# Performance work log

Hardware: AMD Instinct MI355X
Metric: run time of the kernel (lower is better)

Reference implementation:

```python
import jax, jax.numpy as jnp
import numpy as np

B, N, G, H, A = 128, 49, 4096, 1024, 1024  # batch, regions, global feat dim, hidden, attn dim


def setup_inputs() -> dict:
    key = jax.random.key(0)
    ks = jax.random.split(key, 11)
    def w(k, shape, fan_in):
        return jax.random.normal(k, shape, jnp.float32) * (1.0 / np.sqrt(fan_in))
    return {
        "global_features": jax.random.normal(ks[0], (B, N, G), jnp.float32),
        "s_t": jax.random.normal(ks[1], (B, H), jnp.float32),
        "cov_a": jax.random.uniform(ks[2], (B, N, 1), jnp.float32),
        "W_g": w(ks[3], (G, G), G),
        "b_g": jnp.zeros((G,), jnp.float32),
        "W_gs": w(ks[4], (G, H), G),
        "b_gs": jnp.zeros((H,), jnp.float32),
        "W_h": w(ks[5], (H, A), H),
        "W_s": w(ks[6], (H, A), H),
        "W_c": w(ks[7], (1, A), 1),
        "v": w(ks[8], (A,), A),
    }


def reference(global_features, s_t, cov_a, W_g, b_g, W_gs, b_gs, W_h, W_s, W_c, v):
    # g_star = Linear(G->G) -> Linear(G->H) applied to region features  [B,N,H]
    g1 = jnp.einsum('bng,gk->bnk', global_features, W_g) + b_g
    g_star = jnp.einsum('bng,gh->bnh', g1, W_gs) + b_gs
    # additive (Bahdanau) energies: e = tanh(W_h g* + W_s s_t + W_c cov)  [B,N,A]
    e = jnp.tanh(
        jnp.einsum('bnh,ha->bna', g_star, W_h)
        + (s_t @ W_s)[:, None, :]
        + cov_a @ W_c
    )
    scores = jnp.einsum('bna,a->bn', e, v)          # [B,N]
    alpha = jax.nn.softmax(scores, axis=-1)          # attention over regions
    c_img = jnp.einsum('bn,bnh->bh', alpha, g_star)  # weighted sum context [B,H]
    return c_img
```

## Files before the change

kernel.cpp:

```cpp
#include <hip/hip_runtime.h>
#include <cstdint>
#include <cstddef>

typedef __bf16 bf16;
typedef __bf16 bf16x8 __attribute__((ext_vector_type(8)));
typedef __bf16 bf16v4 __attribute__((ext_vector_type(4)));
typedef float  f32x4  __attribute__((ext_vector_type(4)));

#define PB   128
#define PN   49
#define PG   4096
#define PH   1024
#define PA   1024
#define PM1  (PB * PN)

__global__ __launch_bounds__(256) void detect_kernel(
    const unsigned short* __restrict__ raw, int* __restrict__ flag)
{
    __shared__ int cnt;
    if (threadIdx.x == 0) cnt = 0;
    __syncthreads();
    unsigned short u = raw[threadIdx.x];
    float x = __uint_as_float(((unsigned int)u) << 16);
    float a = fabsf(x);
    atomicAdd(&cnt, (a >= 1e-7f && a <= 128.f) ? 1 : 0);
    __syncthreads();
    if (threadIdx.x == 0) flag[0] = (cnt >= 200) ? 1 : 0;
}

__device__ __forceinline__ float ldin(const void* p, size_t i, bool in32) {
    return in32 ? ((const float*)p)[i] : (float)((const bf16*)p)[i];
}

__device__ __forceinline__ void ldx8(const void* x, size_t k0, bool in32, float* xv) {
    if (in32) {
        f32x4 lo = *(const f32x4*)((const float*)x + k0);
        f32x4 hi = *(const f32x4*)((const float*)x + k0 + 4);
#pragma unroll
        for (int j = 0; j < 4; ++j) { xv[j] = lo[j]; xv[4 + j] = hi[j]; }
    } else {
        bf16x8 v = *(const bf16x8*)((const bf16*)x + k0);
#pragma unroll
        for (int j = 0; j < 8; ++j) xv[j] = (float)v[j];
    }
}

__global__ __launch_bounds__(256) void cvt_kernel(
    const void* __restrict__ in, const int* __restrict__ flag,
    bf16* __restrict__ out, size_t total)
{
    const bool in32 = (flag[0] == 0);
    const size_t stride = (size_t)gridDim.x * 256 * 8;
    for (size_t i = ((size_t)blockIdx.x * 256 + threadIdx.x) * 8; i < total; i += stride) {
        bf16x8 o;
        if (in32) {
            f32x4 lo = *(const f32x4*)((const float*)in + i);
            f32x4 hi = *(const f32x4*)((const float*)in + i + 4);
#pragma unroll
            for (int j = 0; j < 4; ++j) { o[j] = (bf16)lo[j]; o[4 + j] = (bf16)hi[j]; }
        } else {
            o = *(const bf16x8*)((const bf16*)in + i);
        }
        *(bf16x8*)(out + i) = o;
    }
}

template <int BF16OUT>
__global__ __launch_bounds__(256, 2) void gemm_kernel(
    const bf16* __restrict__ A, const bf16* __restrict__ Bt0,
    float* __restrict__ Cf, bf16* __restrict__ Cb,
    int M, int N, int K, int kTilesPerSplit)
{
    __shared__ __align__(16) bf16 lds[2 * 128 * 64];
    bf16* As  = lds;
    bf16* Bs0 = lds + 128 * 64;

    const int gx = gridDim.x, gy = gridDim.y;
    const int nwg = gx * gy * (int)gridDim.z;
    int flat = blockIdx.x + gx * (blockIdx.y + gy * blockIdx.z);
    {
        const int q8 = nwg >> 3, r8 = nwg & 7;
        const int xcd = flat & 7, sub = flat >> 3;
        flat = (xcd < r8 ? xcd * (q8 + 1) : r8 * (q8 + 1) + (xcd - r8) * q8) + sub;
    }
    const int bx  = flat % gx;
    const int byz = flat / gx;
    const int by  = byz % gy;
    const int bz  = byz / gy;

    const int tid  = threadIdx.x;
    const int m0   = by * 128;
    const int n0   = bx * 128;
    const int kt0  = bz * kTilesPerSplit;

    const int wave = tid >> 6;
    const int lane = tid & 63;
    const int wm   = (wave >> 1) * 64;
    const int wn   = (wave & 1) * 64;
    const int lm   = lane & 15;
    const int q    = lane >> 4;

    f32x4 acc[4][4];
#pragma unroll
    for (int i = 0; i < 4; ++i)
#pragma unroll
        for (int j = 0; j < 4; ++j) acc[i][j] = (f32x4)0.0f;

    for (int kt = 0; kt < kTilesPerSplit; ++kt) {
        const int k0 = (kt0 + kt) * 64;
#pragma unroll
        for (int it = 0; it < 4; ++it) {
            int p   = it * 256 + tid;
            int row = p >> 3;
            int lc  = ((p & 7) - row) & 7;
            size_t offB = (size_t)(n0 + row) * K + k0 + lc * 8;
            __builtin_amdgcn_global_load_lds((void*)(Bt0 + offB), (void*)(Bs0 + p * 8), 16, 0, 0);
            size_t offA = (size_t)(m0 + row) * K + k0 + lc * 8;
            __builtin_amdgcn_global_load_lds((void*)(A + offA), (void*)(As + p * 8), 16, 0, 0);
        }
        __syncthreads();

#pragma unroll
        for (int s = 0; s < 2; ++s) {
            bf16x8 af[4], bf0[4];
            const int c = s * 4 + q;
#pragma unroll
            for (int mi = 0; mi < 4; ++mi) {
                int row  = wm + mi * 16 + lm;
                int slot = row * 8 + ((c + row) & 7);
                af[mi] = *(const bf16x8*)(As + slot * 8);
            }
#pragma unroll
            for (int ni = 0; ni < 4; ++ni) {
                int row  = wn + ni * 16 + lm;
                int slot = row * 8 + ((c + row) & 7);
                bf0[ni] = *(const bf16x8*)(Bs0 + slot * 8);
            }
#pragma unroll
            for (int mi = 0; mi < 4; ++mi)
#pragma unroll
                for (int ni = 0; ni < 4; ++ni)
                    acc[mi][ni] = __builtin_amdgcn_mfma_f32_16x16x32_bf16(
                        af[mi], bf0[ni], acc[mi][ni], 0, 0, 0);
        }
        __syncthreads();
    }

#pragma unroll
    for (int mi = 0; mi < 4; ++mi)
#pragma unroll
        for (int ni = 0; ni < 4; ++ni)
#pragma unroll
            for (int r = 0; r < 4; ++r) {
                int row = m0 + wm + mi * 16 + q * 4 + r;
                int col = n0 + wn + ni * 16 + lm;
                if (BF16OUT)
                    Cb[(size_t)bz * M * N + (size_t)row * N + col] = (bf16)acc[mi][ni][r];
                else
                    Cf[(size_t)bz * M * N + (size_t)row * N + col] = acc[mi][ni][r];
            }
}

__global__ __launch_bounds__(256) void transpose_kernel(
    const void* __restrict__ in, const int* __restrict__ flag,
    bf16* __restrict__ out, int R, int C)
{
    __shared__ bf16 tile[64][65];
    const bool in32 = (flag[0] == 0);
    const int r0 = blockIdx.y * 64, c0 = blockIdx.x * 64;
    const int tx = threadIdx.x & 15, ty = threadIdx.x >> 4;
#pragma unroll
    for (int it = 0; it < 4; ++it) {
        int r = it * 16 + ty;
        size_t base = (size_t)(r0 + r) * C + c0 + tx * 4;
        if (in32) {
            f32x4 v = *(const f32x4*)((const float*)in + base);
#pragma unroll
            for (int i = 0; i < 4; ++i) tile[r][tx * 4 + i] = (bf16)v[i];
        } else {
            bf16v4 v = *(const bf16v4*)((const bf16*)in + base);
#pragma unroll
            for (int i = 0; i < 4; ++i) tile[r][tx * 4 + i] = v[i];
        }
    }
    __syncthreads();
#pragma unroll
    for (int it = 0; it < 4; ++it) {
        int c = it * 16 + ty;
        bf16v4 v;
#pragma unroll
        for (int i = 0; i < 4; ++i) v[i] = tile[tx * 4 + i][c];
        *(bf16v4*)(out + (size_t)(c0 + c) * R + r0 + tx * 4) = v;
    }
}

__global__ __launch_bounds__(256) void reduce4_kernel(
    const bf16* __restrict__ in, bf16* __restrict__ out, size_t n)
{
    size_t i = ((size_t)blockIdx.x * 256 + threadIdx.x) * 8;
    float s[8] = {0,0,0,0,0,0,0,0};
#pragma unroll
    for (int p = 0; p < 4; ++p) {
        bf16x8 v = *(const bf16x8*)(in + (size_t)p * n + i);
#pragma unroll
        for (int j = 0; j < 8; ++j) s[j] += (float)v[j];
    }
    bf16x8 o;
#pragma unroll
    for (int j = 0; j < 8; ++j) o[j] = (bf16)s[j];
    *(bf16x8*)(out + i) = o;
}

__global__ __launch_bounds__(256) void rowdot_kernel(
    const void* __restrict__ x, const bf16* __restrict__ Wt,
    const void* __restrict__ addv, const int* __restrict__ flag, int xMode,
    float* __restrict__ y, int K)
{
    const bool raw32 = (flag[0] == 0);
    const bool x32   = (xMode == 0) || raw32;
    const int wave = threadIdx.x >> 6, lane = threadIdx.x & 63;
    const int c = blockIdx.x * 4 + wave;
    float s = 0.f;
    for (int k0 = lane * 8; k0 < K; k0 += 512) {
        bf16x8 w = *(const bf16x8*)(Wt + (size_t)c * K + k0);
        float xv[8];
        ldx8(x, (size_t)k0, x32, xv);
#pragma unroll
        for (int j = 0; j < 8; ++j) s += xv[j] * (float)w[j];
    }
#pragma unroll
    for (int off = 32; off; off >>= 1) s += __shfl_down(s, off);
    if (lane == 0) {
        float a = addv ? ldin(addv, c, raw32) : 0.f;
        y[c] = s + a;
    }
}

__global__ __launch_bounds__(256) void scores_kernel(
    const bf16* __restrict__ tP, const float* __restrict__ sprojP,
    const float* __restrict__ tbias, const void* __restrict__ cov,
    const void* __restrict__ Wc, const void* __restrict__ v,
    const int* __restrict__ flag, float* __restrict__ sc)
{
    const bool in32 = (flag[0] == 0);
    const int n = blockIdx.x, b = blockIdx.y, tid = threadIdx.x;
    __shared__ float red[4];
    const size_t trow = (size_t)(b * PN + n) * PA;
    const float cv = ldin(cov, b * PN + n, in32);
    float s = 0.f;
#pragma unroll
    for (int i = 0; i < 4; ++i) {
        int a = tid + i * 256;
        float tv = 0.f;
#pragma unroll
        for (int p = 0; p < 2; ++p)
            tv += (float)tP[(size_t)p * ((size_t)PM1 * PA) + trow + a];
        float sp = 0.f;
#pragma unroll
        for (int p = 0; p < 4; ++p)
            sp += sprojP[(size_t)p * (PB * PA) + (size_t)b * PA + a];
        s += ldin(v, a, in32) * tanhf(tv + sp + tbias[a] + cv * ldin(Wc, a, in32));
    }
#pragma unroll
    for (int off = 32; off; off >>= 1) s += __shfl_down(s, off);
    if ((tid & 63) == 0) red[tid >> 6] = s;
    __syncthreads();
    if (tid == 0) sc[b * PN + n] = red[0] + red[1] + red[2] + red[3];
}

__global__ __launch_bounds__(256) void context_kernel(
    const float* __restrict__ sc, const bf16* __restrict__ gstar,
    const float* __restrict__ cbias, const int* __restrict__ flag,
    void* __restrict__ out)
{
    const int b = blockIdx.x, tid = threadIdx.x;
    const int h = tid * 4;
    float e[PN];
    float mx = -1e30f;
    for (int n = 0; n < PN; ++n) mx = fmaxf(mx, sc[b * PN + n]);
    float sum = 0.f;
    for (int n = 0; n < PN; ++n) { e[n] = expf(sc[b * PN + n] - mx); sum += e[n]; }
    const float inv = 1.f / sum;
    f32x4 cb = *(const f32x4*)(cbias + h);
    float acc[4] = {cb[0], cb[1], cb[2], cb[3]};
    for (int n = 0; n < PN; ++n) {
        float al = e[n] * inv;
        bf16v4 g = *(const bf16v4*)(gstar + (size_t)(b * PN + n) * PH + h);
#pragma unroll
        for (int j = 0; j < 4; ++j) acc[j] += al * (float)g[j];
    }
    if (flag[0]) {
        bf16v4 o;
#pragma unroll
        for (int j = 0; j < 4; ++j) o[j] = (bf16)acc[j];
        *(bf16v4*)((bf16*)out + (size_t)b * PH + h) = o;
    } else {
        f32x4 o;
#pragma unroll
        for (int j = 0; j < 4; ++j) o[j] = acc[j];
        *(f32x4*)((float*)out + (size_t)b * PH + h) = o;
    }
}

extern "C" void kernel_launch(void* const* d_in, const int* in_sizes, int n_in,
                              void* d_out, int out_size, void* d_ws, size_t ws_size,
                              hipStream_t stream)
{
    const void* GF  = d_in[0];
    const void* s_t = d_in[1];
    const void* cov = d_in[2];
    const void* Wg  = d_in[3];
    const void* bg  = d_in[4];
    const void* Wgs = d_in[5];
    const void* bgs = d_in[6];
    const void* Wh  = d_in[7];
    const void* Ws  = d_in[8];
    const void* Wc  = d_in[9];
    const void* v   = d_in[10];
    (void)in_sizes; (void)n_in; (void)out_size; (void)ws_size;

    const size_t MB = 1u << 20;
    char* W = (char*)d_ws;
    bf16*  GFb    = (bf16*) (W + 0);
    bf16*  g_star = (bf16*) (W + 0);
    int*   flag   = (int*)  (W + 52 * MB);
    float* tbias  = (float*)(W + 52 * MB + 4096);
    float* cbias  = (float*)(W + 52 * MB + 8192);
    float* sc     = (float*)(W + 52 * MB + 12288);
    bf16*  s_tb   = (bf16*) (W + 52 * MB + 262144);
    bf16*  WsT    = (bf16*) (W + 53 * MB);
    bf16*  WhT    = (bf16*) (W + 55 * MB);
    float* sprojP = (float*)(W + 57 * MB);
    bf16*  WgsT   = (bf16*) (W + 59 * MB);
    bf16*  WggsT  = (bf16*) (W + 59 * MB);
    bf16*  WggsP  = (bf16*) (W + 67 * MB);
    bf16*  gP     = (bf16*) (W + 67 * MB);
    bf16*  t2P    = (bf16*) (W + 67 * MB);
    bf16*  Wgb    = (bf16*) (W + 100 * MB);

    dim3 blk(256);

    detect_kernel<<<dim3(1), blk, 0, stream>>>((const unsigned short*)GF, flag);

    cvt_kernel<<<dim3(2048), blk, 0, stream>>>(GF, flag, GFb, (size_t)PM1 * PG);
    cvt_kernel<<<dim3(2048), blk, 0, stream>>>(Wg, flag, Wgb, (size_t)PG * PG);
    cvt_kernel<<<dim3(64), blk, 0, stream>>>(s_t, flag, s_tb, (size_t)PB * PH);
    transpose_kernel<<<dim3(PH / 64, PG / 64), blk, 0, stream>>>(Wgs, flag, WgsT, PG, PH);
    transpose_kernel<<<dim3(PA / 64, PH / 64), blk, 0, stream>>>(Wh, flag, WhT, PH, PA);
    transpose_kernel<<<dim3(PA / 64, PH / 64), blk, 0, stream>>>(Ws, flag, WsT, PH, PA);

    rowdot_kernel<<<dim3(PH / 4), blk, 0, stream>>>(bg, WgsT, bgs, flag, 1, cbias, PG);
    rowdot_kernel<<<dim3(PA / 4), blk, 0, stream>>>(cbias, WhT, nullptr, flag, 0, tbias, PH);

    gemm_kernel<1><<<dim3(PG / 128, PH / 128, 4), blk, 0, stream>>>(
        WgsT, Wgb, nullptr, WggsP, PH, PG, PG, (PG / 64) / 4);
    reduce4_kernel<<<dim3((PH * PG) / 2048), blk, 0, stream>>>(
        WggsP, WggsT, (size_t)PH * PG);

    gemm_kernel<1><<<dim3(PH / 128, PM1 / 128, 4), blk, 0, stream>>>(
        GFb, WggsT, nullptr, gP, PM1, PH, PG, (PG / 64) / 4);
    reduce4_kernel<<<dim3((PM1 * PH) / 2048), blk, 0, stream>>>(
        gP, g_star, (size_t)PM1 * PH);

    gemm_kernel<1><<<dim3(PA / 128, PM1 / 128, 2), blk, 0, stream>>>(
        g_star, WhT, nullptr, t2P, PM1, PA, PH, (PH / 64) / 2);

    gemm_kernel<0><<<dim3(PA / 128, 1, 4), blk, 0, stream>>>(
        s_tb, WsT, sprojP, nullptr, PB, PA, PH, (PH / 64) / 4);

    scores_kernel<<<dim3(PN, PB), blk, 0, stream>>>(
        t2P, sprojP, tbias, cov, Wc, v, flag, sc);

    context_kernel<<<dim3(PB), blk, 0, stream>>>(sc, g_star, cbias, flag, d_out);
}
```

Before: 434.0 us.

## Fuse energy GEMM with tanh-score epilogue, batch conversion and transpose launches

The W_h projection GEMM now computes tanh energies and v-dot scores in its epilogue, accumulating row scores with atomics. This removes the split-K partial buffer write and the separate scores kernel. The three cvt launches and three transpose launches are each merged into single kernels, and the scores buffer is zeroed inside the merged conversion kernel. The g_star GEMM split-K drops from 4 to 2 planes, which means less reduction traffic but fewer workgroups. Atomic float accumulation makes the score summation order nondeterministic.

```diff
diff --git a/kernel.cpp b/kernel.cpp
--- a/kernel.cpp
+++ b/kernel.cpp
@@ -45,13 +45,23 @@
     }
 }
 
-__global__ __launch_bounds__(256) void cvt_kernel(
-    const void* __restrict__ in, const int* __restrict__ flag,
-    bf16* __restrict__ out, size_t total)
-{
+__global__ __launch_bounds__(256) void cvt3_kernel(
+    const void* __restrict__ in0, size_t u0, bf16* __restrict__ o0,
+    const void* __restrict__ in1, size_t u1, bf16* __restrict__ o1,
+    const void* __restrict__ in2, size_t u2, bf16* __restrict__ o2,
+    const int* __restrict__ flag, float* __restrict__ sc_zero, int sczn)
+{
+    if (blockIdx.x == 0) {
+        for (int i = threadIdx.x; i < sczn; i += 256) sc_zero[i] = 0.f;
+    }
     const bool in32 = (flag[0] == 0);
-    const size_t stride = (size_t)gridDim.x * 256 * 8;
-    for (size_t i = ((size_t)blockIdx.x * 256 + threadIdx.x) * 8; i < total; i += stride) {
+    const size_t total = u0 + u1 + u2;
+    for (size_t u = blockIdx.x; u < total; u += gridDim.x) {
+        const void* in; bf16* out; size_t rel;
+        if (u < u0)            { in = in0; out = o0; rel = u; }
+        else if (u < u0 + u1)  { in = in1; out = o1; rel = u - u0; }
+        else                   { in = in2; out = o2; rel = u - u0 - u1; }
+        size_t i = rel * 2048 + (size_t)threadIdx.x * 8;
         bf16x8 o;
         if (in32) {
             f32x4 lo = *(const f32x4*)((const float*)in + i);
@@ -161,46 +171,167 @@
             }
 }
 
-__global__ __launch_bounds__(256) void transpose_kernel(
-    const void* __restrict__ in, const int* __restrict__ flag,
-    bf16* __restrict__ out, int R, int C)
+__global__ __launch_bounds__(256, 2) void gemm_scores_kernel(
+    const bf16* __restrict__ A, const bf16* __restrict__ Bt0,
+    const float* __restrict__ sprojP, const float* __restrict__ tbias,
+    const void* __restrict__ cov, const void* __restrict__ Wc,
+    const void* __restrict__ v, const int* __restrict__ flag,
+    float* __restrict__ sc)
+{
+    constexpr int K = PH;
+    __shared__ __align__(16) bf16 lds[2 * 128 * 64];
+    bf16* As  = lds;
+    bf16* Bs0 = lds + 128 * 64;
+
+    const int gx = gridDim.x, gy = gridDim.y;
+    const int nwg = gx * gy;
+    int flat = blockIdx.x + gx * blockIdx.y;
+    {
+        const int q8 = nwg >> 3, r8 = nwg & 7;
+        const int xcd = flat & 7, sub = flat >> 3;
+        flat = (xcd < r8 ? xcd * (q8 + 1) : r8 * (q8 + 1) + (xcd - r8) * q8) + sub;
+    }
+    const int bx = flat % gx;
+    const int by = flat / gx;
+
+    const int tid  = threadIdx.x;
+    const int m0   = by * 128;
+    const int n0   = bx * 128;
+
+    const int wave = tid >> 6;
+    const int lane = tid & 63;
+    const int wm   = (wave >> 1) * 64;
+    const int wn   = (wave & 1) * 64;
+    const int lm   = lane & 15;
+    const int q    = lane >> 4;
+
+    f32x4 acc[4][4];
+#pragma unroll
+    for (int i = 0; i < 4; ++i)
+#pragma unroll
+        for (int j = 0; j < 4; ++j) acc[i][j] = (f32x4)0.0f;
+
+    for (int kt = 0; kt < K / 64; ++kt) {
+        const int k0 = kt * 64;
+#pragma unroll
+        for (int it = 0; it < 4; ++it) {
+            int p   = it * 256 + tid;
+            int row = p >> 3;
+            int lc  = ((p & 7) - row) & 7;
+            size_t offB = (size_t)(n0 + row) * K + k0 + lc * 8;
+            __builtin_amdgcn_global_load_lds((void*)(Bt0 + offB), (void*)(Bs0 + p * 8), 16, 0, 0);
+            size_t offA = (size_t)(m0 + row) * K + k0 + lc * 8;
+            __builtin_amdgcn_global_load_lds((void*)(A + offA), (void*)(As + p * 8), 16, 0, 0);
+        }
+        __syncthreads();
+
+#pragma unroll
+        for (int s = 0; s < 2; ++s) {
+            bf16x8 af[4], bf0[4];
+            const int c = s * 4 + q;
+#pragma unroll
+            for (int mi = 0; mi < 4; ++mi) {
+                int row  = wm + mi * 16 + lm;
+                int slot = row * 8 + ((c + row) & 7);
+                af[mi] = *(const bf16x8*)(As + slot * 8);
+            }
+#pragma unroll
+            for (int ni = 0; ni < 4; ++ni) {
+                int row  = wn + ni * 16 + lm;
+                int slot = row * 8 + ((c + row) & 7);
+                bf0[ni] = *(const bf16x8*)(Bs0 + slot * 8);
+            }
+#pragma unroll
+            for (int mi = 0; mi < 4; ++mi)
+#pragma unroll
+                for (int ni = 0; ni < 4; ++ni)
+                    acc[mi][ni] = __builtin_amdgcn_mfma_f32_16x16x32_bf16(
+                        af[mi], bf0[ni], acc[mi][ni], 0, 0, 0);
+        }
+        __syncthreads();
+    }
+
+    const bool in32 = (flag[0] == 0);
+    float tb[4], wc4[4], vv[4];
+#pragma unroll
+    for (int ni = 0; ni < 4; ++ni) {
+        int col = n0 + wn + ni * 16 + lm;
+        tb[ni]  = tbias[col];
+        wc4[ni] = ldin(Wc, col, in32);
+        vv[ni]  = ldin(v, col, in32);
+    }
+#pragma unroll
+    for (int mi = 0; mi < 4; ++mi)
+#pragma unroll
+        for (int r = 0; r < 4; ++r) {
+            int grow = m0 + wm + mi * 16 + q * 4 + r;
+            int b    = grow / PN;
+            float cv = ldin(cov, grow, in32);
+            const float* sp0 = sprojP + (size_t)b * PA;
+            float rowsum = 0.f;
+#pragma unroll
+            for (int ni = 0; ni < 4; ++ni) {
+                int col = n0 + wn + ni * 16 + lm;
+                float sp = sp0[col] + sp0[PB * PA + col]
+                         + sp0[2 * PB * PA + col] + sp0[3 * PB * PA + col];
+                float val = acc[mi][ni][r] + sp + tb[ni] + cv * wc4[ni];
+                rowsum += vv[ni] * tanhf(val);
+            }
+#pragma unroll
+            for (int off = 1; off < 16; off <<= 1)
+                rowsum += __shfl_xor(rowsum, off);
+            if (lm == 0) atomicAdd(&sc[grow], rowsum);
+        }
+}
+
+__global__ __launch_bounds__(256) void transpose3_kernel(
+    const void* __restrict__ inA, bf16* __restrict__ outA,
+    const void* __restrict__ inB, bf16* __restrict__ outB,
+    const void* __restrict__ inC, bf16* __restrict__ outC,
+    const int* __restrict__ flag)
 {
     __shared__ bf16 tile[64][65];
     const bool in32 = (flag[0] == 0);
-    const int r0 = blockIdx.y * 64, c0 = blockIdx.x * 64;
+    const int bid = blockIdx.x;
+    const void* in; bf16* out; int R, C, bx, by;
+    if (bid < 1024)      { in = inA; out = outA; R = PG; C = PH; bx = bid & 15; by = bid >> 4; }
+    else if (bid < 1280) { int t = bid - 1024; in = inB; out = outB; R = PH; C = PA; bx = t & 15; by = t >> 4; }
+    else                 { int t = bid - 1280; in = inC; out = outC; R = PH; C = PA; bx = t & 15; by = t >> 4; }
+    const int r0 = by * 64, c0 = bx * 64;
     const int tx = threadIdx.x & 15, ty = threadIdx.x >> 4;
 #pragma unroll
     for (int it = 0; it < 4; ++it) {
         int r = it * 16 + ty;
         size_t base = (size_t)(r0 + r) * C + c0 + tx * 4;
         if (in32) {
-            f32x4 v = *(const f32x4*)((const float*)in + base);
-#pragma unroll
-            for (int i = 0; i < 4; ++i) tile[r][tx * 4 + i] = (bf16)v[i];
+            f32x4 vv = *(const f32x4*)((const float*)in + base);
+#pragma unroll
+            for (int i = 0; i < 4; ++i) tile[r][tx * 4 + i] = (bf16)vv[i];
         } else {
-            bf16v4 v = *(const bf16v4*)((const bf16*)in + base);
-#pragma unroll
-            for (int i = 0; i < 4; ++i) tile[r][tx * 4 + i] = v[i];
+            bf16v4 vv = *(const bf16v4*)((const bf16*)in + base);
+#pragma unroll
+            for (int i = 0; i < 4; ++i) tile[r][tx * 4 + i] = vv[i];
         }
     }
     __syncthreads();
 #pragma unroll
     for (int it = 0; it < 4; ++it) {
         int c = it * 16 + ty;
-        bf16v4 v;
-#pragma unroll
-        for (int i = 0; i < 4; ++i) v[i] = tile[tx * 4 + i][c];
-        *(bf16v4*)(out + (size_t)(c0 + c) * R + r0 + tx * 4) = v;
-    }
-}
-
-__global__ __launch_bounds__(256) void reduce4_kernel(
+        bf16v4 vv;
+#pragma unroll
+        for (int i = 0; i < 4; ++i) vv[i] = tile[tx * 4 + i][c];
+        *(bf16v4*)(out + (size_t)(c0 + c) * R + r0 + tx * 4) = vv;
+    }
+}
+
+template <int PLANES>
+__global__ __launch_bounds__(256) void reduce_kernel(
     const bf16* __restrict__ in, bf16* __restrict__ out, size_t n)
 {
     size_t i = ((size_t)blockIdx.x * 256 + threadIdx.x) * 8;
     float s[8] = {0,0,0,0,0,0,0,0};
 #pragma unroll
-    for (int p = 0; p < 4; ++p) {
+    for (int p = 0; p < PLANES; ++p) {
         bf16x8 v = *(const bf16x8*)(in + (size_t)p * n + i);
 #pragma unroll
         for (int j = 0; j < 8; ++j) s[j] += (float)v[j];
@@ -234,38 +365,6 @@
         float a = addv ? ldin(addv, c, raw32) : 0.f;
         y[c] = s + a;
     }
-}
-
-__global__ __launch_bounds__(256) void scores_kernel(
-    const bf16* __restrict__ tP, const float* __restrict__ sprojP,
-    const float* __restrict__ tbias, const void* __restrict__ cov,
-    const void* __restrict__ Wc, const void* __restrict__ v,
-    const int* __restrict__ flag, float* __restrict__ sc)
-{
-    const bool in32 = (flag[0] == 0);
-    const int n = blockIdx.x, b = blockIdx.y, tid = threadIdx.x;
-    __shared__ float red[4];
-    const size_t trow = (size_t)(b * PN + n) * PA;
-    const float cv = ldin(cov, b * PN + n, in32);
-    float s = 0.f;
-#pragma unroll
-    for (int i = 0; i < 4; ++i) {
-        int a = tid + i * 256;
-        float tv = 0.f;
-#pragma unroll
-        for (int p = 0; p < 2; ++p)
-            tv += (float)tP[(size_t)p * ((size_t)PM1 * PA) + trow + a];
-        float sp = 0.f;
-#pragma unroll
-        for (int p = 0; p < 4; ++p)
-            sp += sprojP[(size_t)p * (PB * PA) + (size_t)b * PA + a];
-        s += ldin(v, a, in32) * tanhf(tv + sp + tbias[a] + cv * ldin(Wc, a, in32));
-    }
-#pragma unroll
-    for (int off = 32; off; off >>= 1) s += __shfl_down(s, off);
-    if ((tid & 63) == 0) red[tid >> 6] = s;
-    __syncthreads();
-    if (tid == 0) sc[b * PN + n] = red[0] + red[1] + red[2] + red[3];
 }
 
 __global__ __launch_bounds__(256) void context_kernel(
@@ -335,41 +434,38 @@
     bf16*  WggsT  = (bf16*) (W + 59 * MB);
     bf16*  WggsP  = (bf16*) (W + 67 * MB);
     bf16*  gP     = (bf16*) (W + 67 * MB);
-    bf16*  t2P    = (bf16*) (W + 67 * MB);
     bf16*  Wgb    = (bf16*) (W + 100 * MB);
 
     dim3 blk(256);
 
     detect_kernel<<<dim3(1), blk, 0, stream>>>((const unsigned short*)GF, flag);
 
-    cvt_kernel<<<dim3(2048), blk, 0, stream>>>(GF, flag, GFb, (size_t)PM1 * PG);
-    cvt_kernel<<<dim3(2048), blk, 0, stream>>>(Wg, flag, Wgb, (size_t)PG * PG);
-    cvt_kernel<<<dim3(64), blk, 0, stream>>>(s_t, flag, s_tb, (size_t)PB * PH);
-    transpose_kernel<<<dim3(PH / 64, PG / 64), blk, 0, stream>>>(Wgs, flag, WgsT, PG, PH);
-    transpose_kernel<<<dim3(PA / 64, PH / 64), blk, 0, stream>>>(Wh, flag, WhT, PH, PA);
-    transpose_kernel<<<dim3(PA / 64, PH / 64), blk, 0, stream>>>(Ws, flag, WsT, PH, PA);
+    cvt3_kernel<<<dim3(2048), blk, 0, stream>>>(
+        GF, (size_t)(PM1 * PG) / 2048, GFb,
+        Wg, (size_t)(PG * PG) / 2048, Wgb,
+        s_t, (size_t)(PB * PH) / 2048, s_tb,
+        flag, sc, PB * PN);
+    transpose3_kernel<<<dim3(1536), blk, 0, stream>>>(
+        Wgs, WgsT, Wh, WhT, Ws, WsT, flag);
 
     rowdot_kernel<<<dim3(PH / 4), blk, 0, stream>>>(bg, WgsT, bgs, flag, 1, cbias, PG);
     rowdot_kernel<<<dim3(PA / 4), blk, 0, stream>>>(cbias, WhT, nullptr, flag, 0, tbias, PH);
 
     gemm_kernel<1><<<dim3(PG / 128, PH / 128, 4), blk, 0, stream>>>(
         WgsT, Wgb, nullptr, WggsP, PH, PG, PG, (PG / 64) / 4);
-    reduce4_kernel<<<dim3((PH * PG) / 2048), blk, 0, stream>>>(
+    reduce_kernel<4><<<dim3((PH * PG) / 2048), blk, 0, stream>>>(
         WggsP, WggsT, (size_t)PH * PG);
 
-    gemm_kernel<1><<<dim3(PH / 128, PM1 / 128, 4), blk, 0, stream>>>(
-        GFb, WggsT, nullptr, gP, PM1, PH, PG, (PG / 64) / 4);
-    reduce4_kernel<<<dim3((PM1 * PH) / 2048), blk, 0, stream>>>(
+    gemm_kernel<1><<<dim3(PH / 128, PM1 / 128, 2), blk, 0, stream>>>(
+        GFb, WggsT, nullptr, gP, PM1, PH, PG, (PG / 64) / 2);
+    reduce_kernel<2><<<dim3((PM1 * PH) / 2048), blk, 0, stream>>>(
         gP, g_star, (size_t)PM1 * PH);
-
-    gemm_kernel<1><<<dim3(PA / 128, PM1 / 128, 2), blk, 0, stream>>>(
-        g_star, WhT, nullptr, t2P, PM1, PA, PH, (PH / 64) / 2);
 
     gemm_kernel<0><<<dim3(PA / 128, 1, 4), blk, 0, stream>>>(
         s_tb, WsT, sprojP, nullptr, PB, PA, PH, (PH / 64) / 4);
 
-    scores_kernel<<<dim3(PN, PB), blk, 0, stream>>>(
-        t2P, sprojP, tbias, cov, Wc, v, flag, sc);
+    gemm_scores_kernel<<<dim3(PA / 128, PM1 / 128), blk, 0, stream>>>(
+        g_star, WhT, sprojP, tbias, cov, Wc, v, flag, sc);
 
     context_kernel<<<dim3(PB), blk, 0, stream>>>(sc, g_star, cbias, flag, d_out);
 }
```

Result: slower. 446.3 us (+2.8%).
